# Kernel optimization log

Hardware: AMD Instinct MI355X
Metric: run time of the kernel (lower is better)

Reference implementation:

```python
import jax, jax.numpy as jnp
import numpy as np

FIXED_SIZE = (160, 160, 160)

def _reference_grid(grid_size):
    # [d1, d2, d3, 3] float32 grid of voxel indices, as in layer_util.get_reference_grid
    ax = [jnp.arange(d, dtype=jnp.float32) for d in grid_size]
    return jnp.stack(jnp.meshgrid(*ax, indexing="ij"), axis=-1)

def _resample_linear(vol, loc):
    # vol: [B, D1, D2, D3]; loc: [B, f1, f2, f3, 3] (voxel coords in vol space)
    B = vol.shape[0]
    dims = vol.shape[1:4]
    max_f = jnp.asarray([d - 1 for d in dims], dtype=loc.dtype)
    max_i = jnp.asarray([d - 1 for d in dims], dtype=jnp.int32)
    locc = jnp.clip(loc, 0.0, max_f)          # clamp to volume bounds
    lo = jnp.floor(locc)
    w = locc - lo                              # trilinear weights in [0,1]
    i0 = lo.astype(jnp.int32)
    i1 = jnp.minimum(i0 + 1, max_i)
    b = jnp.arange(B).reshape(B, 1, 1, 1)
    x0, y0, z0 = i0[..., 0], i0[..., 1], i0[..., 2]
    x1, y1, z1 = i1[..., 0], i1[..., 1], i1[..., 2]
    wx, wy, wz = w[..., 0], w[..., 1], w[..., 2]
    ux, uy, uz = 1.0 - wx, 1.0 - wy, 1.0 - wz
    g = lambda ix, iy, iz: vol[b, ix, iy, iz]  # 8-neighbor gather
    return (g(x0, y0, z0) * ux * uy * uz +
            g(x0, y0, z1) * ux * uy * wz +
            g(x0, y1, z0) * ux * wy * uz +
            g(x0, y1, z1) * ux * wy * wz +
            g(x1, y0, z0) * wx * uy * uz +
            g(x1, y0, z1) * wx * uy * wz +
            g(x1, y1, z0) * wx * wy * uz +
            g(x1, y1, z1) * wx * wy * wz)

def setup_inputs() -> dict:
    key = jax.random.key(0)
    k1, k2 = jax.random.split(key)
    B = 4
    ddf = jax.random.normal(k1, (B,) + FIXED_SIZE + (3,), dtype=jnp.float32)
    image = jax.random.normal(k2, (B,) + FIXED_SIZE, dtype=jnp.float32)
    return {"ddf": ddf, "image": image}

def reference(ddf, image):
    grid_ref = _reference_grid(FIXED_SIZE)[None]      # [1, f1, f2, f3, 3]
    grid_warped = grid_ref + ddf                      # [B, f1, f2, f3, 3]
    return _resample_linear(image, grid_warped)       # [B, f1, f2, f3]
```

## Files before the change

### kernel.cpp

```cpp
#include <hip/hip_runtime.h>

#define D    160
#define D2   (D * D)
#define D3   (D * D * D)
#define NB   4
#define TILE 4
#define HXL  3
#define WINX 11
#define HYL  3
#define WINY 10
#define ZSL  80
#define HZL  4
#define ZWIN 88
#define NROW (WINX * WINY)
#define LDSF (NROW * ZWIN)
#define NSTAGE ((LDSF + 255) / 256)
#define LDSPAD (NSTAGE * 256)
#define TPB  640
#define NWAVE (TPB / 64)
#define TPD  (D / TILE)
#define NTILE (NB * TPD * 2 * TPD)
#define NBLK 512
#define CNT  (NTILE / NBLK)

typedef float f32x2 __attribute__((ext_vector_type(2)));

__device__ __forceinline__ void sid_decode(int sid, int& b, int& xt, int& zl, int& yt) {
    yt = (sid % TPD) * TILE;
    int t = sid / TPD;
    zl = (t & 1) * ZSL;
    t >>= 1;
    xt = (t % TPD) * TILE;
    b  = t / TPD;
}

__device__ __forceinline__ void issue_ddf(const float* __restrict__ ddf, int sid,
                                          int rx, int ry, int zbl,
                                          f32x2& q0, f32x2& q1, f32x2& q2, size_t& vb) {
    int b, xt, zl, yt;
    sid_decode(sid, b, xt, zl, yt);
    vb = (size_t)b * D3 + (size_t)(xt + rx) * D2 + (size_t)(yt + ry) * D + (zl + zbl);
    const f32x2* dp = (const f32x2*)(ddf + vb * 3);
    q0 = __builtin_nontemporal_load(dp + 0);
    q1 = __builtin_nontemporal_load(dp + 1);
    q2 = __builtin_nontemporal_load(dp + 2);
}

__device__ __forceinline__ void issue_stage(const float* __restrict__ image, int sid,
                                            int w, int lane, float* buf) {
    int b, xt, zl, yt;
    sid_decode(sid, b, xt, zl, yt);
    const float* vol = image + (size_t)b * D3;
    for (int k = w; k < NSTAGE; k += NWAVE) {
        int f  = k * 256 + lane * 4;
        int s  = f / ZWIN;
        int zo = f - s * ZWIN;
        int sx = s / WINY;
        int sy = s - sx * WINY;
        int srcx = min(max(xt - HXL + sx, 0), D - 1);
        int srcy = min(max(yt - HYL + sy, 0), D - 1);
        int srcz = min(max(zl - HZL + zo, 0), D - 4);
        const float* g = vol + srcx * D2 + srcy * D + srcz;
        __builtin_amdgcn_global_load_lds(
            (const __attribute__((address_space(1))) void*)g,
            (__attribute__((address_space(3))) void*)(buf + k * 256),
            16, 0, 0);
    }
}

__device__ __forceinline__ void do_iter(
    const float* __restrict__ ddf, const float* __restrict__ image,
    float* __restrict__ out, int& sid, int& it,
    f32x2& qc0, f32x2& qc1, f32x2& qc2,
    f32x2& qn0, f32x2& qn1, f32x2& qn2,
    size_t& vbc, size_t& vbn,
    float* bufc, float* bufn,
    int rx, int ry, int zbl, int w, int lane)
{
    const float maxf = (float)(D - 1);
    int bC, xtC, zlC, ytC;
    sid_decode(sid, bC, xtC, zlC, ytC);
    const float* volC = image + (size_t)bC * D3;
    int gx = xtC + rx, gy = ytC + ry;

    float wxs[2], wys[2], wzs[2];
    int bases[2];
    unsigned flags = 0;
    f32x2 fb00[2] = {}, fb01[2] = {}, fb10[2] = {}, fb11[2] = {};
    unsigned shbits = 0;
    const float dxs[2] = {qc0.x, qc1.y};
    const float dys[2] = {qc0.y, qc2.x};
    const float dzs[2] = {qc1.x, qc2.y};
#pragma unroll
    for (int j = 0; j < 2; ++j) {
        float fx = (float)gx + dxs[j];
        float fy = (float)gy + dys[j];
        float fz = (float)(zlC + zbl + j) + dzs[j];
        fx = fminf(fmaxf(fx, 0.0f), maxf);
        fy = fminf(fmaxf(fy, 0.0f), maxf);
        fz = fminf(fmaxf(fz, 0.0f), maxf);
        int x0 = (int)fx, y0 = (int)fy, z0 = (int)fz;
        wxs[j] = fx - (float)x0;
        wys[j] = fy - (float)y0;
        wzs[j] = fz - (float)z0;
        int sx0 = x0 - (xtC - HXL);
        int sy0 = y0 - (ytC - HYL);
        int sz0 = z0 - (zlC - HZL);
        bool inWin = ((unsigned)sx0 <= (unsigned)(WINX - 2)) &
                     ((unsigned)sy0 <= (unsigned)(WINY - 2)) &
                     ((unsigned)sz0 <= (unsigned)(ZWIN - 2));
        flags |= (unsigned)inWin << j;
        int cx = min(max(sx0, 0), WINX - 2);
        int cy = min(max(sy0, 0), WINY - 2);
        int cz = min(max(sz0, 0), ZWIN - 2);
        bases[j] = (cx * WINY + cy) * ZWIN + cz;
        if (!inWin) {
            int x1 = min(x0 + 1, D - 1);
            int y1 = min(y0 + 1, D - 1);
            int zc = min(z0, D - 2);
            shbits |= (unsigned)(z0 > zc) << j;
            fb00[j] = *(const f32x2*)(volC + x0 * D2 + y0 * D + zc);
            fb01[j] = *(const f32x2*)(volC + x0 * D2 + y1 * D + zc);
            fb10[j] = *(const f32x2*)(volC + x1 * D2 + y0 * D + zc);
            fb11[j] = *(const f32x2*)(volC + x1 * D2 + y1 * D + zc);
        }
    }

    __builtin_amdgcn_sched_barrier(0);

    if (it + 1 < CNT) {
        issue_ddf(ddf, sid + 1, rx, ry, zbl, qn0, qn1, qn2, vbn);
        issue_stage(image, sid + 1, w, lane, bufn);
    }
    __builtin_amdgcn_sched_barrier(0);

    float res[2];
#pragma unroll
    for (int j = 0; j < 2; ++j) {
        int b00 = bases[j];
        float a0 = bufc[b00],                  a1 = bufc[b00 + 1];
        float c0 = bufc[b00 + ZWIN],           c1 = bufc[b00 + ZWIN + 1];
        float e0 = bufc[b00 + WINY * ZWIN],    e1 = bufc[b00 + WINY * ZWIN + 1];
        float g0 = bufc[b00 + (WINY + 1) * ZWIN], g1 = bufc[b00 + (WINY + 1) * ZWIN + 1];
        float wz = wzs[j];
        if (!((flags >> j) & 1)) {
            bool sh = (shbits >> j) & 1;
            a0 = sh ? fb00[j].y : fb00[j].x;  a1 = fb00[j].y;
            c0 = sh ? fb01[j].y : fb01[j].x;  c1 = fb01[j].y;
            e0 = sh ? fb10[j].y : fb10[j].x;  e1 = fb10[j].y;
            g0 = sh ? fb11[j].y : fb11[j].x;  g1 = fb11[j].y;
        }
        float wx = wxs[j], wy = wys[j];
        float ux = 1.0f - wx, uy = 1.0f - wy, uz = 1.0f - wz;
        res[j] = (a0 * uz + a1 * wz) * (ux * uy)
               + (c0 * uz + c1 * wz) * (ux * wy)
               + (e0 * uz + e1 * wz) * (wx * uy)
               + (g0 * uz + g1 * wz) * (wx * wy);
    }
    f32x2 o = {res[0], res[1]};
    __builtin_nontemporal_store(o, (f32x2*)(out + vbc));

    asm volatile("s_waitcnt vmcnt(1)" ::: "memory");
    __builtin_amdgcn_sched_barrier(0);
    __builtin_amdgcn_s_barrier();
    __builtin_amdgcn_sched_barrier(0);
    ++sid; ++it;
}

__global__ __launch_bounds__(TPB) void warp_kernel(
    const float* __restrict__ ddf,
    const float* __restrict__ image,
    float* __restrict__ out)
{
    extern __shared__ float lds[];
    float* buf0 = lds;
    float* buf1 = lds + LDSPAD;

    int g   = blockIdx.x;
    int gx8 = (g & 7) * (NBLK / 8) + (g >> 3);
    int sid = gx8 * CNT;

    const int tid  = threadIdx.x;
    const int w    = tid >> 6;
    const int lane = tid & 63;
    const int row  = tid / 40;
    const int zbl  = (tid - row * 40) * 2;
    const int rx   = row >> 2, ry = row & 3;

    f32x2 qA0, qA1, qA2, qB0, qB1, qB2;
    size_t vbA = 0, vbB = 0;

    issue_ddf(ddf, sid, rx, ry, zbl, qA0, qA1, qA2, vbA);
    issue_stage(image, sid, w, lane, buf0);
    asm volatile("s_waitcnt vmcnt(0)" ::: "memory");
    __builtin_amdgcn_sched_barrier(0);
    __builtin_amdgcn_s_barrier();
    __builtin_amdgcn_sched_barrier(0);

    int it = 0;
    for (;;) {
        do_iter(ddf, image, out, sid, it, qA0, qA1, qA2, qB0, qB1, qB2,
                vbA, vbB, buf0, buf1, rx, ry, zbl, w, lane);
        if (it >= CNT) break;
        do_iter(ddf, image, out, sid, it, qB0, qB1, qB2, qA0, qA1, qA2,
                vbB, vbA, buf1, buf0, rx, ry, zbl, w, lane);
        if (it >= CNT) break;
    }
}

extern "C" void kernel_launch(void* const* d_in, const int* in_sizes, int n_in,
                              void* d_out, int out_size, void* d_ws, size_t ws_size,
                              hipStream_t stream) {
    const float* ddf   = (const float*)d_in[0];
    const float* image = (const float*)d_in[1];
    float* out = (float*)d_out;

    hipFuncSetAttribute((const void*)warp_kernel,
                        hipFuncAttributeMaxDynamicSharedMemorySize,
                        2 * LDSPAD * (int)sizeof(float));

    warp_kernel<<<NBLK, TPB, 2 * LDSPAD * sizeof(float), stream>>>(ddf, image, out);
}
```

Measured before the change: 101.7 us.

## Halve z-slab per tile, one voxel per thread, and precompute staging indices

Result: slower. 128.3 us (+26.2%).

```diff
diff --git a/kernel.cpp b/kernel.cpp
--- a/kernel.cpp
+++ b/kernel.cpp
@@ -9,18 +9,20 @@
 #define WINX 11
 #define HYL  3
 #define WINY 10
-#define ZSL  80
+#define ZSL  40
 #define HZL  4
-#define ZWIN 88
+#define ZWIN 48
 #define NROW (WINX * WINY)
 #define LDSF (NROW * ZWIN)
 #define NSTAGE ((LDSF + 255) / 256)
 #define LDSPAD (NSTAGE * 256)
 #define TPB  640
 #define NWAVE (TPB / 64)
+#define KMAX ((NSTAGE + NWAVE - 1) / NWAVE)
 #define TPD  (D / TILE)
-#define NTILE (NB * TPD * 2 * TPD)
-#define NBLK 512
+#define NZS  (D / ZSL)
+#define NTILE (NB * TPD * NZS * TPD)
+#define NBLK 1280
 #define CNT  (NTILE / NBLK)
 
 typedef float f32x2 __attribute__((ext_vector_type(2)));
@@ -28,137 +30,120 @@
 __device__ __forceinline__ void sid_decode(int sid, int& b, int& xt, int& zl, int& yt) {
     yt = (sid % TPD) * TILE;
     int t = sid / TPD;
-    zl = (t & 1) * ZSL;
-    t >>= 1;
+    zl = (t & (NZS - 1)) * ZSL;
+    t >>= 2;
     xt = (t % TPD) * TILE;
     b  = t / TPD;
 }
 
 __device__ __forceinline__ void issue_ddf(const float* __restrict__ ddf, int sid,
-                                          int rx, int ry, int zbl,
-                                          f32x2& q0, f32x2& q1, f32x2& q2, size_t& vb) {
+                                          int rx, int ry, int zloc,
+                                          float& dx, float& dy, float& dz, int& vb) {
     int b, xt, zl, yt;
     sid_decode(sid, b, xt, zl, yt);
-    vb = (size_t)b * D3 + (size_t)(xt + rx) * D2 + (size_t)(yt + ry) * D + (zl + zbl);
-    const f32x2* dp = (const f32x2*)(ddf + vb * 3);
-    q0 = __builtin_nontemporal_load(dp + 0);
-    q1 = __builtin_nontemporal_load(dp + 1);
-    q2 = __builtin_nontemporal_load(dp + 2);
+    vb = b * D3 + (xt + rx) * D2 + (yt + ry) * D + (zl + zloc);
+    const float* p = ddf + (size_t)vb * 3;
+    dx = __builtin_nontemporal_load(p);
+    dy = __builtin_nontemporal_load(p + 1);
+    dz = __builtin_nontemporal_load(p + 2);
 }
 
 __device__ __forceinline__ void issue_stage(const float* __restrict__ image, int sid,
-                                            int w, int lane, float* buf) {
+                                            int w, const int* sxp, const int* syp,
+                                            const int* zop, float* buf) {
     int b, xt, zl, yt;
     sid_decode(sid, b, xt, zl, yt);
     const float* vol = image + (size_t)b * D3;
-    for (int k = w; k < NSTAGE; k += NWAVE) {
-        int f  = k * 256 + lane * 4;
-        int s  = f / ZWIN;
-        int zo = f - s * ZWIN;
-        int sx = s / WINY;
-        int sy = s - sx * WINY;
-        int srcx = min(max(xt - HXL + sx, 0), D - 1);
-        int srcy = min(max(yt - HYL + sy, 0), D - 1);
-        int srcz = min(max(zl - HZL + zo, 0), D - 4);
-        const float* g = vol + srcx * D2 + srcy * D + srcz;
-        __builtin_amdgcn_global_load_lds(
-            (const __attribute__((address_space(1))) void*)g,
-            (__attribute__((address_space(3))) void*)(buf + k * 256),
-            16, 0, 0);
+#pragma unroll
+    for (int i = 0; i < KMAX; ++i) {
+        int k = w + i * NWAVE;
+        if (k < NSTAGE) {
+            int srcx = min(max(xt - HXL + sxp[i], 0), D - 1);
+            int srcy = min(max(yt - HYL + syp[i], 0), D - 1);
+            int srcz = min(max(zl - HZL + zop[i], 0), D - 4);
+            const float* g = vol + srcx * D2 + srcy * D + srcz;
+            __builtin_amdgcn_global_load_lds(
+                (const __attribute__((address_space(1))) void*)g,
+                (__attribute__((address_space(3))) void*)(buf + k * 256),
+                16, 0, 0);
+        }
     }
 }
 
 __device__ __forceinline__ void do_iter(
     const float* __restrict__ ddf, const float* __restrict__ image,
     float* __restrict__ out, int& sid, int& it,
-    f32x2& qc0, f32x2& qc1, f32x2& qc2,
-    f32x2& qn0, f32x2& qn1, f32x2& qn2,
-    size_t& vbc, size_t& vbn,
+    float& dxc, float& dyc, float& dzc,
+    float& dxn, float& dyn, float& dzn,
+    int& vbc, int& vbn,
     float* bufc, float* bufn,
-    int rx, int ry, int zbl, int w, int lane)
+    int rx, int ry, int zloc, int w,
+    const int* sxp, const int* syp, const int* zop)
 {
     const float maxf = (float)(D - 1);
     int bC, xtC, zlC, ytC;
     sid_decode(sid, bC, xtC, zlC, ytC);
     const float* volC = image + (size_t)bC * D3;
-    int gx = xtC + rx, gy = ytC + ry;
-
-    float wxs[2], wys[2], wzs[2];
-    int bases[2];
-    unsigned flags = 0;
-    f32x2 fb00[2] = {}, fb01[2] = {}, fb10[2] = {}, fb11[2] = {};
-    unsigned shbits = 0;
-    const float dxs[2] = {qc0.x, qc1.y};
-    const float dys[2] = {qc0.y, qc2.x};
-    const float dzs[2] = {qc1.x, qc2.y};
-#pragma unroll
-    for (int j = 0; j < 2; ++j) {
-        float fx = (float)gx + dxs[j];
-        float fy = (float)gy + dys[j];
-        float fz = (float)(zlC + zbl + j) + dzs[j];
-        fx = fminf(fmaxf(fx, 0.0f), maxf);
-        fy = fminf(fmaxf(fy, 0.0f), maxf);
-        fz = fminf(fmaxf(fz, 0.0f), maxf);
-        int x0 = (int)fx, y0 = (int)fy, z0 = (int)fz;
-        wxs[j] = fx - (float)x0;
-        wys[j] = fy - (float)y0;
-        wzs[j] = fz - (float)z0;
-        int sx0 = x0 - (xtC - HXL);
-        int sy0 = y0 - (ytC - HYL);
-        int sz0 = z0 - (zlC - HZL);
-        bool inWin = ((unsigned)sx0 <= (unsigned)(WINX - 2)) &
-                     ((unsigned)sy0 <= (unsigned)(WINY - 2)) &
-                     ((unsigned)sz0 <= (unsigned)(ZWIN - 2));
-        flags |= (unsigned)inWin << j;
-        int cx = min(max(sx0, 0), WINX - 2);
-        int cy = min(max(sy0, 0), WINY - 2);
-        int cz = min(max(sz0, 0), ZWIN - 2);
-        bases[j] = (cx * WINY + cy) * ZWIN + cz;
-        if (!inWin) {
-            int x1 = min(x0 + 1, D - 1);
-            int y1 = min(y0 + 1, D - 1);
-            int zc = min(z0, D - 2);
-            shbits |= (unsigned)(z0 > zc) << j;
-            fb00[j] = *(const f32x2*)(volC + x0 * D2 + y0 * D + zc);
-            fb01[j] = *(const f32x2*)(volC + x0 * D2 + y1 * D + zc);
-            fb10[j] = *(const f32x2*)(volC + x1 * D2 + y0 * D + zc);
-            fb11[j] = *(const f32x2*)(volC + x1 * D2 + y1 * D + zc);
-        }
+
+    float fx = (float)(xtC + rx) + dxc;
+    float fy = (float)(ytC + ry) + dyc;
+    float fz = (float)(zlC + zloc) + dzc;
+    fx = fminf(fmaxf(fx, 0.0f), maxf);
+    fy = fminf(fmaxf(fy, 0.0f), maxf);
+    fz = fminf(fmaxf(fz, 0.0f), maxf);
+    int x0 = (int)fx, y0 = (int)fy, z0 = (int)fz;
+    float wx = fx - (float)x0;
+    float wy = fy - (float)y0;
+    float wz = fz - (float)z0;
+
+    int sx0 = x0 - xtC + HXL;
+    int sy0 = y0 - ytC + HYL;
+    int sz0 = z0 - zlC + HZL;
+    bool inWin = ((unsigned)sx0 <= (unsigned)(WINX - 2)) &
+                 ((unsigned)sy0 <= (unsigned)(WINY - 2)) &
+                 ((unsigned)sz0 <= (unsigned)(ZWIN - 2));
+    int cx = min(max(sx0, 0), WINX - 2);
+    int cy = min(max(sy0, 0), WINY - 2);
+    int cz = min(max(sz0, 0), ZWIN - 2);
+    int base00 = (cx * WINY + cy) * ZWIN + cz;
+
+    f32x2 fb00 = {}, fb01 = {}, fb10 = {}, fb11 = {};
+    bool sh = false;
+    if (!inWin) {
+        int x1 = min(x0 + 1, D - 1);
+        int y1 = min(y0 + 1, D - 1);
+        int zc = min(z0, D - 2);
+        sh = z0 > zc;
+        fb00 = *(const f32x2*)(volC + x0 * D2 + y0 * D + zc);
+        fb01 = *(const f32x2*)(volC + x0 * D2 + y1 * D + zc);
+        fb10 = *(const f32x2*)(volC + x1 * D2 + y0 * D + zc);
+        fb11 = *(const f32x2*)(volC + x1 * D2 + y1 * D + zc);
     }
 
     __builtin_amdgcn_sched_barrier(0);
 
     if (it + 1 < CNT) {
-        issue_ddf(ddf, sid + 1, rx, ry, zbl, qn0, qn1, qn2, vbn);
-        issue_stage(image, sid + 1, w, lane, bufn);
-    }
-    __builtin_amdgcn_sched_barrier(0);
-
-    float res[2];
-#pragma unroll
-    for (int j = 0; j < 2; ++j) {
-        int b00 = bases[j];
-        float a0 = bufc[b00],                  a1 = bufc[b00 + 1];
-        float c0 = bufc[b00 + ZWIN],           c1 = bufc[b00 + ZWIN + 1];
-        float e0 = bufc[b00 + WINY * ZWIN],    e1 = bufc[b00 + WINY * ZWIN + 1];
-        float g0 = bufc[b00 + (WINY + 1) * ZWIN], g1 = bufc[b00 + (WINY + 1) * ZWIN + 1];
-        float wz = wzs[j];
-        if (!((flags >> j) & 1)) {
-            bool sh = (shbits >> j) & 1;
-            a0 = sh ? fb00[j].y : fb00[j].x;  a1 = fb00[j].y;
-            c0 = sh ? fb01[j].y : fb01[j].x;  c1 = fb01[j].y;
-            e0 = sh ? fb10[j].y : fb10[j].x;  e1 = fb10[j].y;
-            g0 = sh ? fb11[j].y : fb11[j].x;  g1 = fb11[j].y;
-        }
-        float wx = wxs[j], wy = wys[j];
-        float ux = 1.0f - wx, uy = 1.0f - wy, uz = 1.0f - wz;
-        res[j] = (a0 * uz + a1 * wz) * (ux * uy)
-               + (c0 * uz + c1 * wz) * (ux * wy)
-               + (e0 * uz + e1 * wz) * (wx * uy)
-               + (g0 * uz + g1 * wz) * (wx * wy);
-    }
-    f32x2 o = {res[0], res[1]};
-    __builtin_nontemporal_store(o, (f32x2*)(out + vbc));
+        issue_ddf(ddf, sid + 1, rx, ry, zloc, dxn, dyn, dzn, vbn);
+        issue_stage(image, sid + 1, w, sxp, syp, zop, bufn);
+    }
+    __builtin_amdgcn_sched_barrier(0);
+
+    float a0 = bufc[base00],                  a1 = bufc[base00 + 1];
+    float c0 = bufc[base00 + ZWIN],           c1 = bufc[base00 + ZWIN + 1];
+    float e0 = bufc[base00 + WINY * ZWIN],    e1 = bufc[base00 + WINY * ZWIN + 1];
+    float g0 = bufc[base00 + (WINY + 1) * ZWIN], g1 = bufc[base00 + (WINY + 1) * ZWIN + 1];
+    if (!inWin) {
+        a0 = sh ? fb00.y : fb00.x;  a1 = fb00.y;
+        c0 = sh ? fb01.y : fb01.x;  c1 = fb01.y;
+        e0 = sh ? fb10.y : fb10.x;  e1 = fb10.y;
+        g0 = sh ? fb11.y : fb11.x;  g1 = fb11.y;
+    }
+    float ux = 1.0f - wx, uy = 1.0f - wy, uz = 1.0f - wz;
+    float res = (a0 * uz + a1 * wz) * (ux * uy)
+              + (c0 * uz + c1 * wz) * (ux * wy)
+              + (e0 * uz + e1 * wz) * (wx * uy)
+              + (g0 * uz + g1 * wz) * (wx * wy);
+    __builtin_nontemporal_store(res, out + vbc);
 
     asm volatile("s_waitcnt vmcnt(1)" ::: "memory");
     __builtin_amdgcn_sched_barrier(0);
@@ -184,14 +169,25 @@
     const int w    = tid >> 6;
     const int lane = tid & 63;
     const int row  = tid / 40;
-    const int zbl  = (tid - row * 40) * 2;
+    const int zloc = tid - row * 40;
     const int rx   = row >> 2, ry = row & 3;
 
-    f32x2 qA0, qA1, qA2, qB0, qB1, qB2;
-    size_t vbA = 0, vbB = 0;
-
-    issue_ddf(ddf, sid, rx, ry, zbl, qA0, qA1, qA2, vbA);
-    issue_stage(image, sid, w, lane, buf0);
+    int sxp[KMAX], syp[KMAX], zop[KMAX];
+#pragma unroll
+    for (int i = 0; i < KMAX; ++i) {
+        int k = w + i * NWAVE;
+        int f = k * 256 + lane * 4;
+        int s = f / ZWIN;
+        zop[i] = f - s * ZWIN;
+        sxp[i] = s / WINY;
+        syp[i] = s - sxp[i] * WINY;
+    }
+
+    float dxA, dyA, dzA, dxB, dyB, dzB;
+    int vbA = 0, vbB = 0;
+
+    issue_ddf(ddf, sid, rx, ry, zloc, dxA, dyA, dzA, vbA);
+    issue_stage(image, sid, w, sxp, syp, zop, buf0);
     asm volatile("s_waitcnt vmcnt(0)" ::: "memory");
     __builtin_amdgcn_sched_barrier(0);
     __builtin_amdgcn_s_barrier();
@@ -199,11 +195,11 @@
 
     int it = 0;
     for (;;) {
-        do_iter(ddf, image, out, sid, it, qA0, qA1, qA2, qB0, qB1, qB2,
-                vbA, vbB, buf0, buf1, rx, ry, zbl, w, lane);
+        do_iter(ddf, image, out, sid, it, dxA, dyA, dzA, dxB, dyB, dzB,
+                vbA, vbB, buf0, buf1, rx, ry, zloc, w, sxp, syp, zop);
         if (it >= CNT) break;
-        do_iter(ddf, image, out, sid, it, qB0, qB1, qB2, qA0, qA1, qA2,
-                vbB, vbA, buf1, buf0, rx, ry, zbl, w, lane);
+        do_iter(ddf, image, out, sid, it, dxB, dyB, dzB, dxA, dyA, dzA,
+                vbB, vbA, buf1, buf0, rx, ry, zloc, w, sxp, syp, zop);
         if (it >= CNT) break;
     }
 }
@@ -215,9 +211,5 @@
     const float* image = (const float*)d_in[1];
     float* out = (float*)d_out;
 
-    hipFuncSetAttribute((const void*)warp_kernel,
-                        hipFuncAttributeMaxDynamicSharedMemorySize,
-                        2 * LDSPAD * (int)sizeof(float));
-
     warp_kernel<<<NBLK, TPB, 2 * LDSPAD * sizeof(float), stream>>>(ddf, image, out);
 }
```

## Retile to 8x8x20 output tiles with precomputed staging addresses sweeping along y

Applied to the files above, without the earlier changes.

New measurement: 146.0 us. +43.6%, slower.

```diff
diff --git a/kernel.cpp b/kernel.cpp
--- a/kernel.cpp
+++ b/kernel.cpp
@@ -4,98 +4,77 @@
 #define D2   (D * D)
 #define D3   (D * D * D)
 #define NB   4
-#define TILE 4
+#define TX   8
+#define TY   8
+#define ZSL  20
 #define HXL  3
-#define WINX 11
+#define WINX 15
 #define HYL  3
-#define WINY 10
-#define ZSL  80
+#define WINY 14
 #define HZL  4
-#define ZWIN 88
+#define ZWIN 28
 #define NROW (WINX * WINY)
 #define LDSF (NROW * ZWIN)
 #define NSTAGE ((LDSF + 255) / 256)
 #define LDSPAD (NSTAGE * 256)
 #define TPB  640
 #define NWAVE (TPB / 64)
-#define TPD  (D / TILE)
-#define NTILE (NB * TPD * 2 * TPD)
-#define NBLK 512
+#define TPDX (D / TX)
+#define TPDY (D / TY)
+#define NZS  (D / ZSL)
+#define NTILE (NB * TPDX * NZS * TPDY)
+#define NBLK 1280
 #define CNT  (NTILE / NBLK)
+#define BASECLAMP (((WINX-2) * WINY + (WINY-2)) * ZWIN + (ZWIN-2))
 
 typedef float f32x2 __attribute__((ext_vector_type(2)));
 
-__device__ __forceinline__ void sid_decode(int sid, int& b, int& xt, int& zl, int& yt) {
-    yt = (sid % TPD) * TILE;
-    int t = sid / TPD;
-    zl = (t & 1) * ZSL;
-    t >>= 1;
-    xt = (t % TPD) * TILE;
-    b  = t / TPD;
-}
-
-__device__ __forceinline__ void issue_ddf(const float* __restrict__ ddf, int sid,
-                                          int rx, int ry, int zbl,
-                                          f32x2& q0, f32x2& q1, f32x2& q2, size_t& vb) {
-    int b, xt, zl, yt;
-    sid_decode(sid, b, xt, zl, yt);
-    vb = (size_t)b * D3 + (size_t)(xt + rx) * D2 + (size_t)(yt + ry) * D + (zl + zbl);
-    const f32x2* dp = (const f32x2*)(ddf + vb * 3);
-    q0 = __builtin_nontemporal_load(dp + 0);
-    q1 = __builtin_nontemporal_load(dp + 1);
-    q2 = __builtin_nontemporal_load(dp + 2);
-}
-
-__device__ __forceinline__ void issue_stage(const float* __restrict__ image, int sid,
-                                            int w, int lane, float* buf) {
-    int b, xt, zl, yt;
-    sid_decode(sid, b, xt, zl, yt);
-    const float* vol = image + (size_t)b * D3;
-    for (int k = w; k < NSTAGE; k += NWAVE) {
-        int f  = k * 256 + lane * 4;
-        int s  = f / ZWIN;
-        int zo = f - s * ZWIN;
-        int sx = s / WINY;
-        int sy = s - sx * WINY;
-        int srcx = min(max(xt - HXL + sx, 0), D - 1);
-        int srcy = min(max(yt - HYL + sy, 0), D - 1);
-        int srcz = min(max(zl - HZL + zo, 0), D - 4);
-        const float* g = vol + srcx * D2 + srcy * D + srcz;
-        __builtin_amdgcn_global_load_lds(
-            (const __attribute__((address_space(1))) void*)g,
-            (__attribute__((address_space(3))) void*)(buf + k * 256),
-            16, 0, 0);
+struct StageCtx {
+    int pfix[3];
+    int syl[3];
+    int ldof[3];
+    bool have[3];
+};
+
+__device__ __forceinline__ void issue_stage(const float* __restrict__ vol,
+                                            const StageCtx& sc, int yt, float* buf) {
+#pragma unroll
+    for (int i = 0; i < 3; ++i) {
+        if (sc.have[i]) {
+            int srcy = min(max(yt - HYL + sc.syl[i], 0), D - 1);
+            const float* g = vol + sc.pfix[i] + srcy * D;
+            __builtin_amdgcn_global_load_lds(
+                (const __attribute__((address_space(1))) void*)g,
+                (__attribute__((address_space(3))) void*)(buf + sc.ldof[i]),
+                16, 0, 0);
+        }
     }
 }
 
 __device__ __forceinline__ void do_iter(
-    const float* __restrict__ ddf, const float* __restrict__ image,
-    float* __restrict__ out, int& sid, int& it,
-    f32x2& qc0, f32x2& qc1, f32x2& qc2,
-    f32x2& qn0, f32x2& qn1, f32x2& qn2,
-    size_t& vbc, size_t& vbn,
+    const float* __restrict__ vol, const float* __restrict__ ddf,
+    float* __restrict__ out, const StageCtx& sc,
+    int it, int yt, int vb,
+    f32x2 q0, f32x2 q1, f32x2 q2,
+    f32x2& n0, f32x2& n1, f32x2& n2,
     float* bufc, float* bufn,
-    int rx, int ry, int zbl, int w, int lane)
+    float xgf, int zg, int ry, int xwb, int zwb)
 {
     const float maxf = (float)(D - 1);
-    int bC, xtC, zlC, ytC;
-    sid_decode(sid, bC, xtC, zlC, ytC);
-    const float* volC = image + (size_t)bC * D3;
-    int gx = xtC + rx, gy = ytC + ry;
-
+    float ygf = (float)(yt + ry);
+    const float dxs[2] = {q0.x, q1.y};
+    const float dys[2] = {q0.y, q2.x};
+    const float dzs[2] = {q1.x, q2.y};
     float wxs[2], wys[2], wzs[2];
     int bases[2];
-    unsigned flags = 0;
+    unsigned flags = 0, shb = 0;
     f32x2 fb00[2] = {}, fb01[2] = {}, fb10[2] = {}, fb11[2] = {};
-    unsigned shbits = 0;
-    const float dxs[2] = {qc0.x, qc1.y};
-    const float dys[2] = {qc0.y, qc2.x};
-    const float dzs[2] = {qc1.x, qc2.y};
+
 #pragma unroll
     for (int j = 0; j < 2; ++j) {
-        float fx = (float)gx + dxs[j];
-        float fy = (float)gy + dys[j];
-        float fz = (float)(zlC + zbl + j) + dzs[j];
+        float fx = xgf + dxs[j];
+        float fy = ygf + dys[j];
+        float fz = (float)(zg + j) + dzs[j];
         fx = fminf(fmaxf(fx, 0.0f), maxf);
         fy = fminf(fmaxf(fy, 0.0f), maxf);
         fz = fminf(fmaxf(fz, 0.0f), maxf);
@@ -103,34 +82,34 @@
         wxs[j] = fx - (float)x0;
         wys[j] = fy - (float)y0;
         wzs[j] = fz - (float)z0;
-        int sx0 = x0 - (xtC - HXL);
-        int sy0 = y0 - (ytC - HYL);
-        int sz0 = z0 - (zlC - HZL);
+        int sx0 = x0 - xwb, sy0 = y0 - (yt - HYL), sz0 = z0 - zwb;
         bool inWin = ((unsigned)sx0 <= (unsigned)(WINX - 2)) &
                      ((unsigned)sy0 <= (unsigned)(WINY - 2)) &
                      ((unsigned)sz0 <= (unsigned)(ZWIN - 2));
         flags |= (unsigned)inWin << j;
-        int cx = min(max(sx0, 0), WINX - 2);
-        int cy = min(max(sy0, 0), WINY - 2);
-        int cz = min(max(sz0, 0), ZWIN - 2);
-        bases[j] = (cx * WINY + cy) * ZWIN + cz;
+        int base = (sx0 * WINY + sy0) * ZWIN + sz0;
+        bases[j] = (int)min((unsigned)base & 8191u, (unsigned)BASECLAMP);
         if (!inWin) {
             int x1 = min(x0 + 1, D - 1);
             int y1 = min(y0 + 1, D - 1);
             int zc = min(z0, D - 2);
-            shbits |= (unsigned)(z0 > zc) << j;
-            fb00[j] = *(const f32x2*)(volC + x0 * D2 + y0 * D + zc);
-            fb01[j] = *(const f32x2*)(volC + x0 * D2 + y1 * D + zc);
-            fb10[j] = *(const f32x2*)(volC + x1 * D2 + y0 * D + zc);
-            fb11[j] = *(const f32x2*)(volC + x1 * D2 + y1 * D + zc);
+            shb |= (unsigned)(z0 > zc) << j;
+            fb00[j] = *(const f32x2*)(vol + x0 * D2 + y0 * D + zc);
+            fb01[j] = *(const f32x2*)(vol + x0 * D2 + y1 * D + zc);
+            fb10[j] = *(const f32x2*)(vol + x1 * D2 + y0 * D + zc);
+            fb11[j] = *(const f32x2*)(vol + x1 * D2 + y1 * D + zc);
         }
     }
 
     __builtin_amdgcn_sched_barrier(0);
 
     if (it + 1 < CNT) {
-        issue_ddf(ddf, sid + 1, rx, ry, zbl, qn0, qn1, qn2, vbn);
-        issue_stage(image, sid + 1, w, lane, bufn);
+        int vbn = vb + TY * D;
+        const f32x2* dp = (const f32x2*)(ddf + (size_t)vbn * 3);
+        n0 = __builtin_nontemporal_load(dp + 0);
+        n1 = __builtin_nontemporal_load(dp + 1);
+        n2 = __builtin_nontemporal_load(dp + 2);
+        issue_stage(vol, sc, yt + TY, bufn);
     }
     __builtin_amdgcn_sched_barrier(0);
 
@@ -138,19 +117,18 @@
 #pragma unroll
     for (int j = 0; j < 2; ++j) {
         int b00 = bases[j];
-        float a0 = bufc[b00],                  a1 = bufc[b00 + 1];
-        float c0 = bufc[b00 + ZWIN],           c1 = bufc[b00 + ZWIN + 1];
-        float e0 = bufc[b00 + WINY * ZWIN],    e1 = bufc[b00 + WINY * ZWIN + 1];
+        float a0 = bufc[b00],                     a1 = bufc[b00 + 1];
+        float c0 = bufc[b00 + ZWIN],              c1 = bufc[b00 + ZWIN + 1];
+        float e0 = bufc[b00 + WINY * ZWIN],       e1 = bufc[b00 + WINY * ZWIN + 1];
         float g0 = bufc[b00 + (WINY + 1) * ZWIN], g1 = bufc[b00 + (WINY + 1) * ZWIN + 1];
-        float wz = wzs[j];
         if (!((flags >> j) & 1)) {
-            bool sh = (shbits >> j) & 1;
+            bool sh = (shb >> j) & 1;
             a0 = sh ? fb00[j].y : fb00[j].x;  a1 = fb00[j].y;
             c0 = sh ? fb01[j].y : fb01[j].x;  c1 = fb01[j].y;
             e0 = sh ? fb10[j].y : fb10[j].x;  e1 = fb10[j].y;
             g0 = sh ? fb11[j].y : fb11[j].x;  g1 = fb11[j].y;
         }
-        float wx = wxs[j], wy = wys[j];
+        float wx = wxs[j], wy = wys[j], wz = wzs[j];
         float ux = 1.0f - wx, uy = 1.0f - wy, uz = 1.0f - wz;
         res[j] = (a0 * uz + a1 * wz) * (ux * uy)
                + (c0 * uz + c1 * wz) * (ux * wy)
@@ -158,13 +136,12 @@
                + (g0 * uz + g1 * wz) * (wx * wy);
     }
     f32x2 o = {res[0], res[1]};
-    __builtin_nontemporal_store(o, (f32x2*)(out + vbc));
+    __builtin_nontemporal_store(o, (f32x2*)(out + vb));
 
     asm volatile("s_waitcnt vmcnt(1)" ::: "memory");
     __builtin_amdgcn_sched_barrier(0);
     __builtin_amdgcn_s_barrier();
     __builtin_amdgcn_sched_barrier(0);
-    ++sid; ++it;
 }
 
 __global__ __launch_bounds__(TPB) void warp_kernel(
@@ -178,33 +155,73 @@
 
     int g   = blockIdx.x;
     int gx8 = (g & 7) * (NBLK / 8) + (g >> 3);
-    int sid = gx8 * CNT;
+    int yi0 = (gx8 & 1) * CNT;
+    int bxz = gx8 >> 1;
+    int zi  = bxz & (NZS - 1);
+    int t2  = bxz >> 3;
+    int xi  = t2 % TPDX;
+    int b   = t2 / TPDX;
 
     const int tid  = threadIdx.x;
     const int w    = tid >> 6;
     const int lane = tid & 63;
-    const int row  = tid / 40;
-    const int zbl  = (tid - row * 40) * 2;
-    const int rx   = row >> 2, ry = row & 3;
+    const int row  = tid / 10;
+    const int zc   = tid - row * 10;
+    const int zbl  = zc * 2;
+    const int rx   = row >> 3, ry = row & 7;
+
+    const int xg = xi * TX + rx;
+    const int zg = zi * ZSL + zbl;
+    const int xwb = xi * TX - HXL;
+    const int zwb = zi * ZSL - HZL;
+    const float xgf = (float)xg;
+    const float* vol = image + (size_t)b * D3;
+
+    StageCtx sc;
+#pragma unroll
+    for (int i = 0; i < 3; ++i) {
+        int k = w + i * NWAVE;
+        sc.have[i] = (k < NSTAGE);
+        int kk = sc.have[i] ? k : 0;
+        int f  = kk * 256 + lane * 4;
+        int s  = f / ZWIN;
+        int zo = f - s * ZWIN;
+        int sx = s / WINY;
+        int sy = s - sx * WINY;
+        int srcx = min(max(xi * TX - HXL + sx, 0), D - 1);
+        int srcz = min(max(zi * ZSL - HZL + zo, 0), D - 4);
+        sc.pfix[i] = srcx * D2 + srcz;
+        sc.syl[i]  = sy;
+        sc.ldof[i] = kk * 256;
+    }
+
+    int yt = yi0 * TY;
+    int vb = b * D3 + xg * D2 + (yt + ry) * D + zg;
 
     f32x2 qA0, qA1, qA2, qB0, qB1, qB2;
-    size_t vbA = 0, vbB = 0;
-
-    issue_ddf(ddf, sid, rx, ry, zbl, qA0, qA1, qA2, vbA);
-    issue_stage(image, sid, w, lane, buf0);
-    asm volatile("s_waitcnt vmcnt(0)" ::: "memory");
-    __builtin_amdgcn_sched_barrier(0);
-    __builtin_amdgcn_s_barrier();
-    __builtin_amdgcn_sched_barrier(0);
-
-    int it = 0;
-    for (;;) {
-        do_iter(ddf, image, out, sid, it, qA0, qA1, qA2, qB0, qB1, qB2,
-                vbA, vbB, buf0, buf1, rx, ry, zbl, w, lane);
-        if (it >= CNT) break;
-        do_iter(ddf, image, out, sid, it, qB0, qB1, qB2, qA0, qA1, qA2,
-                vbB, vbA, buf1, buf0, rx, ry, zbl, w, lane);
-        if (it >= CNT) break;
+
+    {
+        const f32x2* dp = (const f32x2*)(ddf + (size_t)vb * 3);
+        qA0 = __builtin_nontemporal_load(dp + 0);
+        qA1 = __builtin_nontemporal_load(dp + 1);
+        qA2 = __builtin_nontemporal_load(dp + 2);
+        issue_stage(vol, sc, yt, buf0);
+        asm volatile("s_waitcnt vmcnt(0)" ::: "memory");
+        __builtin_amdgcn_sched_barrier(0);
+        __builtin_amdgcn_s_barrier();
+        __builtin_amdgcn_sched_barrier(0);
+    }
+
+#pragma unroll 1
+    for (int it = 0; it < CNT; it += 2) {
+        do_iter(vol, ddf, out, sc, it, yt, vb,
+                qA0, qA1, qA2, qB0, qB1, qB2, buf0, buf1,
+                xgf, zg, ry, xwb, zwb);
+        yt += TY; vb += TY * D;
+        do_iter(vol, ddf, out, sc, it + 1, yt, vb,
+                qB0, qB1, qB2, qA0, qA1, qA2, buf1, buf0,
+                xgf, zg, ry, xwb, zwb);
+        yt += TY; vb += TY * D;
     }
 }
 
@@ -215,9 +232,5 @@
     const float* image = (const float*)d_in[1];
     float* out = (float*)d_out;
 
-    hipFuncSetAttribute((const void*)warp_kernel,
-                        hipFuncAttributeMaxDynamicSharedMemorySize,
-                        2 * LDSPAD * (int)sizeof(float));
-
     warp_kernel<<<NBLK, TPB, 2 * LDSPAD * sizeof(float), stream>>>(ddf, image, out);
 }
```
